# Kernel tuning notes

Hardware: AMD Instinct MI355X
Metric: run time of the kernel (lower is better)

## Reference

```python
import jax, jax.numpy as jnp
import numpy as np

N = 8192
IN_DIM = 512
OUT_DIM = 64
ALPHA = 0.2  # LeakyReLU negative slope
NEG_FILL = -9e15


def setup_inputs() -> dict:
    key = jax.random.key(0)
    k1, k2, k3, k4 = jax.random.split(key, 4)
    features = jax.random.normal(k1, (N, IN_DIM), dtype=jnp.float32)
    adj = jax.random.randint(k2, (N, N), 0, 2, dtype=jnp.int32)
    # xavier_normal with gain 1.414 ~ sqrt(2)
    W = jax.random.normal(k3, (IN_DIM, OUT_DIM), dtype=jnp.float32) * (1.414 * np.sqrt(2.0 / (IN_DIM + OUT_DIM)))
    a = jax.random.normal(k4, (2 * OUT_DIM, 1), dtype=jnp.float32) * (1.414 * np.sqrt(2.0 / (2 * OUT_DIM + 1)))
    return {"features": features, "adj": adj, "W": W, "a": a}


def reference(features, adj, W, a):
    h = features @ W                      # [N, OUT_DIM]
    h1 = h @ a[:OUT_DIM, :]               # [N, 1]
    h2 = h @ a[OUT_DIM:, :]               # [N, 1]
    e = h1 + h2.T                         # [N, N] broadcast add
    e = jnp.where(e > 0, e, ALPHA * e)    # LeakyReLU
    scores = jnp.where(adj > 0, e, NEG_FILL)
    attention = jax.nn.softmax(scores, axis=-1)
    out = attention @ h                   # [N, OUT_DIM]
    out = jax.nn.elu(out)                 # concat=True branch
    return out
```

## Files before the change

### kernel.cpp

```cpp
#include <hip/hip_runtime.h>
#include <hip/hip_bf16.h>

#define N 8192
#define IN_DIM 512
#define OUT_DIM 64
#define ALPHA 0.2f
#define LOG2E 1.44269504f

typedef __hip_bfloat16 bf16;
typedef __attribute__((ext_vector_type(8))) short bf16x8;
typedef __attribute__((ext_vector_type(4))) float f32x4;
typedef __attribute__((ext_vector_type(4))) int   int4v;
typedef __attribute__((ext_vector_type(4))) float float4v;

__device__ __forceinline__ float u2f(unsigned short u) {
    union { unsigned int i; float f; } c; c.i = ((unsigned int)u) << 16; return c.f;
}

__device__ __forceinline__ uint2 splitpack2(float f0, float f1) {
    unsigned u0 = __float_as_uint(f0), u1 = __float_as_uint(f1);
    unsigned h0 = u0 & 0xFFFF0000u, h1 = u1 & 0xFFFF0000u;
    float l0 = f0 - __uint_as_float(h0);
    float l1 = f1 - __uint_as_float(h1);
    uint2 r;
    r.x = (h0 >> 16) | h1;
    r.y = (__float_as_uint(l0) >> 16) | (__float_as_uint(l1) & 0xFFFF0000u);
    return r;
}

__device__ __forceinline__ bf16x8 as_bf16x8(int a, int b, int c, int d) {
    union { int4v i; bf16x8 b; } u;
    u.i = (int4v){a, b, c, d};
    return u.b;
}

__device__ __forceinline__ unsigned fenc(float f) {
    unsigned u = __float_as_uint(f);
    return (u & 0x80000000u) ? ~u : (u | 0x80000000u);
}
__device__ __forceinline__ float fdec(unsigned e) {
    return (e & 0x80000000u) ? __uint_as_float(e & 0x7FFFFFFFu) : __uint_as_float(~e);
}

__device__ __forceinline__ int4v ntload4(const int* p) {
    return __builtin_nontemporal_load((const int4v*)p);
}

__global__ __launch_bounds__(256) void k_prep(const unsigned short* __restrict__ feat_u16,
                                              const void* __restrict__ Wv,
                                              int* __restrict__ flag,
                                              unsigned short* __restrict__ WT_hi,
                                              unsigned short* __restrict__ WT_lo,
                                              unsigned* __restrict__ h2enc) {
    __shared__ int sflag;
    int tid = threadIdx.x;
    if (tid < 64) {
        float v = u2f(feat_u16[2 * tid]);
        float av = fabsf(v);
        int ok = (v == 0.f) || (av > 1e-8f && av < 1e8f);
        unsigned long long m = __ballot(ok);
        if (tid == 0) sflag = (__popcll(m) >= 48) ? 1 : 0;
    }
    __syncthreads();
    int isbf = sflag;
    if (blockIdx.x == 0 && tid == 0) { *flag = isbf; *h2enc = fenc(-3e38f); }
    int idx = blockIdx.x * 256 + tid;
    int k = idx >> 6, c = idx & 63;
    float w = isbf ? u2f(((const unsigned short*)Wv)[idx]) : ((const float*)Wv)[idx];
    unsigned u = __float_as_uint(w);
    unsigned hi = u & 0xFFFF0000u;
    float lo = w - __uint_as_float(hi);
    WT_hi[c * IN_DIM + k] = (unsigned short)(hi >> 16);
    WT_lo[c * IN_DIM + k] = (unsigned short)(__float_as_uint(lo) >> 16);
}

__global__ __launch_bounds__(256) void k_h(const void* __restrict__ featv,
                                           const unsigned short* __restrict__ WT_hi,
                                           const unsigned short* __restrict__ WT_lo,
                                           const void* __restrict__ av,
                                           const int* __restrict__ flag,
                                           float* __restrict__ h1,
                                           float* __restrict__ h2,
                                           unsigned short* __restrict__ hT_hi,
                                           unsigned short* __restrict__ hT_lo,
                                           unsigned* __restrict__ h2enc) {
    __shared__ float C[16][66];
    const int tid = threadIdx.x;
    const int wave = tid >> 6;
    const int lane = tid & 63;
    const int rsub = lane & 15;
    const int g = lane >> 4;
    const int wrow0 = blockIdx.x * 16;
    const int isbf = *flag;

    f32x4 acc0 = {0.f,0.f,0.f,0.f}, acc1 = {0.f,0.f,0.f,0.f};
    f32x4 acc2 = {0.f,0.f,0.f,0.f}, acc3 = {0.f,0.f,0.f,0.f};

    const int kbeg = wave * (IN_DIM / 4);
    for (int k0 = kbeg; k0 < kbeg + IN_DIM / 4; k0 += 32) {
        const int ka = k0 + g * 8;
        bf16x8 Ah, Al;
        if (isbf) {
            Ah = *(const bf16x8*)((const unsigned short*)featv + (size_t)(wrow0 + rsub) * IN_DIM + ka);
            Al = as_bf16x8(0, 0, 0, 0);
        } else {
            const float* fp = (const float*)featv + (size_t)(wrow0 + rsub) * IN_DIM + ka;
            float4v f0 = *(const float4v*)fp;
            float4v f1 = *(const float4v*)(fp + 4);
            uint2 q0 = splitpack2(f0[0], f0[1]);
            uint2 q1 = splitpack2(f0[2], f0[3]);
            uint2 q2 = splitpack2(f1[0], f1[1]);
            uint2 q3 = splitpack2(f1[2], f1[3]);
            Ah = as_bf16x8((int)q0.x, (int)q1.x, (int)q2.x, (int)q3.x);
            Al = as_bf16x8((int)q0.y, (int)q1.y, (int)q2.y, (int)q3.y);
        }
        const unsigned short* wh = WT_hi + (size_t)rsub * IN_DIM + ka;
        const unsigned short* wl = WT_lo + (size_t)rsub * IN_DIM + ka;
        bf16x8 B0h = *(const bf16x8*)(wh);
        bf16x8 B1h = *(const bf16x8*)(wh + 16 * IN_DIM);
        bf16x8 B2h = *(const bf16x8*)(wh + 32 * IN_DIM);
        bf16x8 B3h = *(const bf16x8*)(wh + 48 * IN_DIM);
        bf16x8 B0l = *(const bf16x8*)(wl);
        bf16x8 B1l = *(const bf16x8*)(wl + 16 * IN_DIM);
        bf16x8 B2l = *(const bf16x8*)(wl + 32 * IN_DIM);
        bf16x8 B3l = *(const bf16x8*)(wl + 48 * IN_DIM);

        acc0 = __builtin_amdgcn_mfma_f32_16x16x32_bf16(Ah, B0h, acc0, 0, 0, 0);
        acc1 = __builtin_amdgcn_mfma_f32_16x16x32_bf16(Ah, B1h, acc1, 0, 0, 0);
        acc2 = __builtin_amdgcn_mfma_f32_16x16x32_bf16(Ah, B2h, acc2, 0, 0, 0);
        acc3 = __builtin_amdgcn_mfma_f32_16x16x32_bf16(Ah, B3h, acc3, 0, 0, 0);
        acc0 = __builtin_amdgcn_mfma_f32_16x16x32_bf16(Ah, B0l, acc0, 0, 0, 0);
        acc1 = __builtin_amdgcn_mfma_f32_16x16x32_bf16(Ah, B1l, acc1, 0, 0, 0);
        acc2 = __builtin_amdgcn_mfma_f32_16x16x32_bf16(Ah, B2l, acc2, 0, 0, 0);
        acc3 = __builtin_amdgcn_mfma_f32_16x16x32_bf16(Ah, B3l, acc3, 0, 0, 0);
        acc0 = __builtin_amdgcn_mfma_f32_16x16x32_bf16(Al, B0h, acc0, 0, 0, 0);
        acc1 = __builtin_amdgcn_mfma_f32_16x16x32_bf16(Al, B1h, acc1, 0, 0, 0);
        acc2 = __builtin_amdgcn_mfma_f32_16x16x32_bf16(Al, B2h, acc2, 0, 0, 0);
        acc3 = __builtin_amdgcn_mfma_f32_16x16x32_bf16(Al, B3h, acc3, 0, 0, 0);
    }

    if (wave == 0) {
#pragma unroll
        for (int r = 0; r < 4; ++r) {
            C[g * 4 + r][rsub]      = acc0[r];
            C[g * 4 + r][16 + rsub] = acc1[r];
            C[g * 4 + r][32 + rsub] = acc2[r];
            C[g * 4 + r][48 + rsub] = acc3[r];
        }
    }
    __syncthreads();
#pragma unroll
    for (int w2 = 1; w2 < 4; ++w2) {
        if (wave == w2) {
#pragma unroll
            for (int r = 0; r < 4; ++r) {
                C[g * 4 + r][rsub]      += acc0[r];
                C[g * 4 + r][16 + rsub] += acc1[r];
                C[g * 4 + r][32 + rsub] += acc2[r];
                C[g * 4 + r][48 + rsub] += acc3[r];
            }
        }
        __syncthreads();
    }

    {
        int c = tid >> 2;
        int r0 = (tid & 3) * 4;
        int a = wrow0 + r0;
        int dest = (a & ~31) + 8 * ((a >> 2) & 3) + 4 * ((a >> 4) & 1);
        float v0 = C[r0 + 0][c], v1 = C[r0 + 1][c], v2 = C[r0 + 2][c], v3 = C[r0 + 3][c];
        uint2 s01 = splitpack2(v0, v1);
        uint2 s23 = splitpack2(v2, v3);
        size_t off = (size_t)c * N + dest;
        { uint2 ph; ph.x = s01.x; ph.y = s23.x; *(uint2*)(hT_hi + off) = ph; }
        { uint2 pl; pl.x = s01.y; pl.y = s23.y; *(uint2*)(hT_lo + off) = pl; }
    }

    if (wave == 0 && lane < 16) {
        const float* af = (const float*)av;
        const unsigned short* au = (const unsigned short*)av;
        float s1 = 0.f, s2 = 0.f;
#pragma unroll 8
        for (int c = 0; c < 64; ++c) {
            float a1 = isbf ? u2f(au[c])      : af[c];
            float a2 = isbf ? u2f(au[64 + c]) : af[64 + c];
            float hv = C[lane][c];
            s1 += hv * a1;
            s2 += hv * a2;
        }
        s1 *= LOG2E; s2 *= LOG2E;
        h1[wrow0 + lane] = s1;
        h2[wrow0 + lane] = s2;
        float wm = s2;
#pragma unroll
        for (int off = 8; off; off >>= 1) wm = fmaxf(wm, __shfl_xor(wm, off));
        if (lane == 0) atomicMax(h2enc, fenc(wm));
    }
}

__global__ __launch_bounds__(256, 2) void k_attn(const int* __restrict__ adj,
                                                 const float* __restrict__ h1,
                                                 const float* __restrict__ h2,
                                                 const unsigned short* __restrict__ hT_hi,
                                                 const unsigned short* __restrict__ hT_lo,
                                                 const unsigned* __restrict__ h2enc,
                                                 float* __restrict__ pacc,
                                                 float* __restrict__ plner,
                                                 int klen) {
    __shared__ float accs[64][66];
    __shared__ float lredL[4][64];

    const int wave = threadIdx.x >> 6;
    const int lane = threadIdx.x & 63;
    const int rsub = lane & 15;
    const int g = lane >> 4;
    const int row0 = blockIdx.x * 64;
    const int kbid = blockIdx.y;

    const float h2m = fdec(*h2enc);
    float h1r[4], c0[4];
#pragma unroll
    for (int mt = 0; mt < 4; ++mt) {
        h1r[mt] = h1[row0 + mt * 16 + rsub];
        float u = h1r[mt] + h2m;
        c0[mt] = -fmaxf(u, ALPHA * u);
    }

    f32x4 acc[4][4];
#pragma unroll
    for (int mt = 0; mt < 4; ++mt)
#pragma unroll
        for (int ct = 0; ct < 4; ++ct) acc[mt][ct] = (f32x4){0.f, 0.f, 0.f, 0.f};
    float lacc[4] = {0.f, 0.f, 0.f, 0.f};

    const unsigned short* bph = hT_hi + (size_t)rsub * N;
    const unsigned short* bpl = hT_lo + (size_t)rsub * N;

    const int kbeg = kbid * klen + wave * (klen >> 2);
    const int kend = kbeg + (klen >> 2);
    for (int k0 = kbeg; k0 < kend; k0 += 32) {
        const int kb = k0 + g * 8;
        const int ca = k0 + g * 4;
        const int cb = k0 + 16 + g * 4;

        const unsigned short* bh = bph + kb;
        const unsigned short* bl = bpl + kb;
        bf16x8 B0h = *(const bf16x8*)(bh);
        bf16x8 B1h = *(const bf16x8*)(bh + 16 * (size_t)N);
        bf16x8 B2h = *(const bf16x8*)(bh + 32 * (size_t)N);
        bf16x8 B3h = *(const bf16x8*)(bh + 48 * (size_t)N);
        bf16x8 B0l = *(const bf16x8*)(bl);
        bf16x8 B1l = *(const bf16x8*)(bl + 16 * (size_t)N);
        bf16x8 B2l = *(const bf16x8*)(bl + 32 * (size_t)N);
        bf16x8 B3l = *(const bf16x8*)(bl + 48 * (size_t)N);

        float4v hA = *(const float4v*)(h2 + ca);
        float4v hB = *(const float4v*)(h2 + cb);

#pragma unroll
        for (int mt = 0; mt < 4; ++mt) {
            const size_t arow = (size_t)(row0 + mt * 16 + rsub) * N;
            int4v aj0 = ntload4(adj + arow + ca);
            int4v aj1 = ntload4(adj + arow + cb);

            float w[8];
#pragma unroll
            for (int j = 0; j < 4; ++j) {
                float u = h1r[mt] + hA[j];
                float s = fmaxf(u, ALPHA * u);
                float e = exp2f(s + c0[mt]);
                w[j] = aj0[j] > 0 ? e : 0.f;
            }
#pragma unroll
            for (int j = 0; j < 4; ++j) {
                float u = h1r[mt] + hB[j];
                float s = fmaxf(u, ALPHA * u);
                float e = exp2f(s + c0[mt]);
                w[4 + j] = aj1[j] > 0 ? e : 0.f;
            }
#pragma unroll
            for (int j = 0; j < 8; ++j) lacc[mt] += w[j];

            uint2 p0 = splitpack2(w[0], w[1]);
            uint2 p1 = splitpack2(w[2], w[3]);
            uint2 p2 = splitpack2(w[4], w[5]);
            uint2 p3 = splitpack2(w[6], w[7]);
            bf16x8 Ahi = as_bf16x8((int)p0.x, (int)p1.x, (int)p2.x, (int)p3.x);
            bf16x8 Alo = as_bf16x8((int)p0.y, (int)p1.y, (int)p2.y, (int)p3.y);

            acc[mt][0] = __builtin_amdgcn_mfma_f32_16x16x32_bf16(Ahi, B0h, acc[mt][0], 0, 0, 0);
            acc[mt][1] = __builtin_amdgcn_mfma_f32_16x16x32_bf16(Ahi, B1h, acc[mt][1], 0, 0, 0);
            acc[mt][2] = __builtin_amdgcn_mfma_f32_16x16x32_bf16(Ahi, B2h, acc[mt][2], 0, 0, 0);
            acc[mt][3] = __builtin_amdgcn_mfma_f32_16x16x32_bf16(Ahi, B3h, acc[mt][3], 0, 0, 0);
            acc[mt][0] = __builtin_amdgcn_mfma_f32_16x16x32_bf16(Ahi, B0l, acc[mt][0], 0, 0, 0);
            acc[mt][1] = __builtin_amdgcn_mfma_f32_16x16x32_bf16(Ahi, B1l, acc[mt][1], 0, 0, 0);
            acc[mt][2] = __builtin_amdgcn_mfma_f32_16x16x32_bf16(Ahi, B2l, acc[mt][2], 0, 0, 0);
            acc[mt][3] = __builtin_amdgcn_mfma_f32_16x16x32_bf16(Ahi, B3l, acc[mt][3], 0, 0, 0);
            acc[mt][0] = __builtin_amdgcn_mfma_f32_16x16x32_bf16(Alo, B0h, acc[mt][0], 0, 0, 0);
            acc[mt][1] = __builtin_amdgcn_mfma_f32_16x16x32_bf16(Alo, B1h, acc[mt][1], 0, 0, 0);
            acc[mt][2] = __builtin_amdgcn_mfma_f32_16x16x32_bf16(Alo, B2h, acc[mt][2], 0, 0, 0);
            acc[mt][3] = __builtin_amdgcn_mfma_f32_16x16x32_bf16(Alo, B3h, acc[mt][3], 0, 0, 0);
        }
    }

#pragma unroll
    for (int mt = 0; mt < 4; ++mt) {
        float l = lacc[mt];
        l += __shfl_xor(l, 16);
        l += __shfl_xor(l, 32);
        if (g == 0) lredL[wave][mt * 16 + rsub] = l;
    }

    if (wave == 0) {
#pragma unroll
        for (int mt = 0; mt < 4; ++mt)
#pragma unroll
            for (int ct = 0; ct < 4; ++ct)
#pragma unroll
                for (int r = 0; r < 4; ++r)
                    accs[mt * 16 + g * 4 + r][ct * 16 + rsub] = acc[mt][ct][r];
    }
    __syncthreads();
#pragma unroll
    for (int w2 = 1; w2 < 4; ++w2) {
        if (wave == w2) {
#pragma unroll
            for (int mt = 0; mt < 4; ++mt)
#pragma unroll
                for (int ct = 0; ct < 4; ++ct)
#pragma unroll
                    for (int r = 0; r < 4; ++r)
                        accs[mt * 16 + g * 4 + r][ct * 16 + rsub] += acc[mt][ct][r];
        }
        __syncthreads();
    }

    float* pa = pacc + (size_t)kbid * (N * OUT_DIM);
#pragma unroll
    for (int p = 0; p < 16; ++p) {
        int idx = p * 256 + threadIdx.x;
        int rl = idx >> 6, col = idx & 63;
        pa[(size_t)(row0 + rl) * OUT_DIM + col] = accs[rl][col];
    }
    if (threadIdx.x < 64)
        plner[(size_t)kbid * N + row0 + threadIdx.x] =
            lredL[0][threadIdx.x] + lredL[1][threadIdx.x] + lredL[2][threadIdx.x] + lredL[3][threadIdx.x];
}

__global__ __launch_bounds__(256) void k_out(const float* __restrict__ pacc,
                                             const float* __restrict__ plner,
                                             const int* __restrict__ flag,
                                             void* __restrict__ outv,
                                             int nkb) {
    int idx = blockIdx.x * 256 + threadIdx.x;
    int row = idx >> 6;
    float v = 0.f, l = 0.f;
    for (int kb = 0; kb < nkb; ++kb) {
        v += pacc[(size_t)kb * (N * OUT_DIM) + idx];
        l += plner[(size_t)kb * N + row];
    }
    float o = l > 0.f ? v / l : 0.f;
    o = o > 0.f ? o : exp2f(o * LOG2E) - 1.f;
    if (*flag) ((bf16*)outv)[idx] = __float2bfloat16(o);
    else       ((float*)outv)[idx] = o;
}

extern "C" void kernel_launch(void* const* d_in, const int* in_sizes, int n_in,
                              void* d_out, int out_size, void* d_ws, size_t ws_size,
                              hipStream_t stream) {
    const void* feat = d_in[0];
    const int* adj = (const int*)d_in[1];
    const void* W = d_in[2];
    const void* a = d_in[3];

    char* ws = (char*)d_ws;
    int*      flag  = (int*)(ws);
    unsigned* h2enc = (unsigned*)(ws + 256);
    float* h1       = (float*)(ws + 4096);
    float* h2       = (float*)(ws + 36864);
    unsigned short* hT_hi = (unsigned short*)(ws + 69632);
    unsigned short* hT_lo = (unsigned short*)(ws + 69632 + 1048576);
    unsigned short* WT_hi = (unsigned short*)(ws + 2166784);
    unsigned short* WT_lo = (unsigned short*)(ws + 2166784 + 65536);
    char* dynbase = ws + 2297856;

    size_t cap = ws_size ? ws_size : ((size_t)1 << 30);
    int nkb = 8;
    while (nkb > 1) {
        size_t need = 2297856 + (size_t)nkb * ((size_t)N * OUT_DIM * 4 + (size_t)N * 4);
        if (need <= cap) break;
        nkb >>= 1;
    }
    float* pacc  = (float*)dynbase;
    float* plner = (float*)(dynbase + (size_t)nkb * N * OUT_DIM * 4);

    hipLaunchKernelGGL(k_prep, dim3((IN_DIM * OUT_DIM) / 256), dim3(256), 0, stream,
                       (const unsigned short*)feat, W, flag, WT_hi, WT_lo, h2enc);
    hipLaunchKernelGGL(k_h, dim3(N / 16), dim3(256), 0, stream,
                       feat, WT_hi, WT_lo, a, flag, h1, h2, hT_hi, hT_lo, h2enc);
    hipLaunchKernelGGL(k_attn, dim3(N / 64, nkb), dim3(256), 0, stream,
                       adj, h1, h2, hT_hi, hT_lo, h2enc, pacc, plner, N / nkb);
    hipLaunchKernelGGL(k_out, dim3((N * OUT_DIM) / 256), dim3(256), 0, stream,
                       pacc, plner, flag, d_out, nkb);
}
```

Before: 436.0 us.

## Pack adjacency into bitmask in projection kernel and consume bits in attention

Adds extra blocks to the feature-projection kernel that read the int32 adjacency once and ballot it into a 1-bit-per-entry mask. The attention kernel then stages its rows of the mask in shared memory instead of streaming 4-byte adjacency values from global memory per MFMA step. The hT layout is simplified to plain row order, to match the new column-to-bit mapping. Adjacency is still read in full once, but now in a kernel that overlaps with the projection, and the attention kernel gains LDS usage and a barrier. The number of key splits can no longer drop below four.

```diff
diff --git a/kernel.cpp b/kernel.cpp
--- a/kernel.cpp
+++ b/kernel.cpp
@@ -40,10 +40,6 @@
 }
 __device__ __forceinline__ float fdec(unsigned e) {
     return (e & 0x80000000u) ? __uint_as_float(e & 0x7FFFFFFFu) : __uint_as_float(~e);
-}
-
-__device__ __forceinline__ int4v ntload4(const int* p) {
-    return __builtin_nontemporal_load((const int4v*)p);
 }
 
 __global__ __launch_bounds__(256) void k_prep(const unsigned short* __restrict__ feat_u16,
@@ -74,20 +70,38 @@
     WT_lo[c * IN_DIM + k] = (unsigned short)(__float_as_uint(lo) >> 16);
 }
 
-__global__ __launch_bounds__(256) void k_h(const void* __restrict__ featv,
-                                           const unsigned short* __restrict__ WT_hi,
-                                           const unsigned short* __restrict__ WT_lo,
-                                           const void* __restrict__ av,
-                                           const int* __restrict__ flag,
-                                           float* __restrict__ h1,
-                                           float* __restrict__ h2,
-                                           unsigned short* __restrict__ hT_hi,
-                                           unsigned short* __restrict__ hT_lo,
-                                           unsigned* __restrict__ h2enc) {
+__global__ __launch_bounds__(256) void k_hp(const void* __restrict__ featv,
+                                            const unsigned short* __restrict__ WT_hi,
+                                            const unsigned short* __restrict__ WT_lo,
+                                            const void* __restrict__ av,
+                                            const int* __restrict__ flag,
+                                            float* __restrict__ h1,
+                                            float* __restrict__ h2,
+                                            unsigned short* __restrict__ hT_hi,
+                                            unsigned short* __restrict__ hT_lo,
+                                            unsigned* __restrict__ h2enc,
+                                            const int* __restrict__ adj,
+                                            unsigned* __restrict__ abits) {
     __shared__ float C[16][66];
     const int tid = threadIdx.x;
     const int wave = tid >> 6;
     const int lane = tid & 63;
+
+    if (blockIdx.x >= N / 16) {
+        const size_t base = (size_t)(blockIdx.x - N / 16) * 512;
+#pragma unroll 4
+        for (int it = 0; it < 128; ++it) {
+            size_t chunk = base + (size_t)it * 4 + wave;
+            int v = adj[chunk * 64 + lane];
+            unsigned long long m = __ballot(v > 0);
+            if (lane == 0) {
+                uint2 p; p.x = (unsigned)m; p.y = (unsigned)(m >> 32);
+                *(uint2*)(abits + chunk * 2) = p;
+            }
+        }
+        return;
+    }
+
     const int rsub = lane & 15;
     const int g = lane >> 4;
     const int wrow0 = blockIdx.x * 16;
@@ -166,12 +180,10 @@
     {
         int c = tid >> 2;
         int r0 = (tid & 3) * 4;
-        int a = wrow0 + r0;
-        int dest = (a & ~31) + 8 * ((a >> 2) & 3) + 4 * ((a >> 4) & 1);
         float v0 = C[r0 + 0][c], v1 = C[r0 + 1][c], v2 = C[r0 + 2][c], v3 = C[r0 + 3][c];
         uint2 s01 = splitpack2(v0, v1);
         uint2 s23 = splitpack2(v2, v3);
-        size_t off = (size_t)c * N + dest;
+        size_t off = (size_t)c * N + wrow0 + r0;
         { uint2 ph; ph.x = s01.x; ph.y = s23.x; *(uint2*)(hT_hi + off) = ph; }
         { uint2 pl; pl.x = s01.y; pl.y = s23.y; *(uint2*)(hT_lo + off) = pl; }
     }
@@ -198,7 +210,7 @@
     }
 }
 
-__global__ __launch_bounds__(256, 2) void k_attn(const int* __restrict__ adj,
+__global__ __launch_bounds__(256, 2) void k_attn(const unsigned* __restrict__ abits,
                                                  const float* __restrict__ h1,
                                                  const float* __restrict__ h2,
                                                  const unsigned short* __restrict__ hT_hi,
@@ -209,6 +221,7 @@
                                                  int klen) {
     __shared__ float accs[64][66];
     __shared__ float lredL[4][64];
+    __shared__ unsigned msk[64][65];
 
     const int wave = threadIdx.x >> 6;
     const int lane = threadIdx.x & 63;
@@ -217,6 +230,13 @@
     const int row0 = blockIdx.x * 64;
     const int kbid = blockIdx.y;
 
+    const int wpr = klen >> 5;
+    const int wsh = 31 - __clz(wpr);
+    for (int i = threadIdx.x; i < 64 * wpr; i += 256) {
+        int r = i >> wsh, w = i & (wpr - 1);
+        msk[r][w] = abits[(size_t)(row0 + r) * (N / 32) + (size_t)kbid * wpr + w];
+    }
+
     const float h2m = fdec(*h2enc);
     float h1r[4], c0[4];
 #pragma unroll
@@ -236,12 +256,14 @@
     const unsigned short* bph = hT_hi + (size_t)rsub * N;
     const unsigned short* bpl = hT_lo + (size_t)rsub * N;
 
+    __syncthreads();
+
     const int kbeg = kbid * klen + wave * (klen >> 2);
     const int kend = kbeg + (klen >> 2);
+    const int sh = g * 8;
     for (int k0 = kbeg; k0 < kend; k0 += 32) {
         const int kb = k0 + g * 8;
-        const int ca = k0 + g * 4;
-        const int cb = k0 + 16 + g * 4;
+        const int wi = (k0 - kbid * klen) >> 5;
 
         const unsigned short* bh = bph + kb;
         const unsigned short* bl = bpl + kb;
@@ -254,14 +276,12 @@
         bf16x8 B2l = *(const bf16x8*)(bl + 32 * (size_t)N);
         bf16x8 B3l = *(const bf16x8*)(bl + 48 * (size_t)N);
 
-        float4v hA = *(const float4v*)(h2 + ca);
-        float4v hB = *(const float4v*)(h2 + cb);
+        float4v hA = *(const float4v*)(h2 + kb);
+        float4v hB = *(const float4v*)(h2 + kb + 4);
 
 #pragma unroll
         for (int mt = 0; mt < 4; ++mt) {
-            const size_t arow = (size_t)(row0 + mt * 16 + rsub) * N;
-            int4v aj0 = ntload4(adj + arow + ca);
-            int4v aj1 = ntload4(adj + arow + cb);
+            const unsigned mask = msk[mt * 16 + rsub][wi];
 
             float w[8];
 #pragma unroll
@@ -269,14 +289,14 @@
                 float u = h1r[mt] + hA[j];
                 float s = fmaxf(u, ALPHA * u);
                 float e = exp2f(s + c0[mt]);
-                w[j] = aj0[j] > 0 ? e : 0.f;
+                w[j] = ((mask >> (sh + j)) & 1u) ? e : 0.f;
             }
 #pragma unroll
             for (int j = 0; j < 4; ++j) {
                 float u = h1r[mt] + hB[j];
                 float s = fmaxf(u, ALPHA * u);
                 float e = exp2f(s + c0[mt]);
-                w[4 + j] = aj1[j] > 0 ? e : 0.f;
+                w[4 + j] = ((mask >> (sh + 4 + j)) & 1u) ? e : 0.f;
             }
 #pragma unroll
             for (int j = 0; j < 8; ++j) lacc[mt] += w[j];
@@ -382,12 +402,13 @@
     unsigned short* hT_lo = (unsigned short*)(ws + 69632 + 1048576);
     unsigned short* WT_hi = (unsigned short*)(ws + 2166784);
     unsigned short* WT_lo = (unsigned short*)(ws + 2166784 + 65536);
-    char* dynbase = ws + 2297856;
+    unsigned* abits = (unsigned*)(ws + 2297856);
+    char* dynbase = ws + 2297856 + (size_t)N * (N / 8);
 
     size_t cap = ws_size ? ws_size : ((size_t)1 << 30);
     int nkb = 8;
-    while (nkb > 1) {
-        size_t need = 2297856 + (size_t)nkb * ((size_t)N * OUT_DIM * 4 + (size_t)N * 4);
+    while (nkb > 4) {
+        size_t need = (size_t)(dynbase - ws) + (size_t)nkb * ((size_t)N * OUT_DIM * 4 + (size_t)N * 4);
         if (need <= cap) break;
         nkb >>= 1;
     }
@@ -396,10 +417,10 @@
 
     hipLaunchKernelGGL(k_prep, dim3((IN_DIM * OUT_DIM) / 256), dim3(256), 0, stream,
                        (const unsigned short*)feat, W, flag, WT_hi, WT_lo, h2enc);
-    hipLaunchKernelGGL(k_h, dim3(N / 16), dim3(256), 0, stream,
-                       feat, WT_hi, WT_lo, a, flag, h1, h2, hT_hi, hT_lo, h2enc);
+    hipLaunchKernelGGL(k_hp, dim3(N / 16 + 2048), dim3(256), 0, stream,
+                       feat, WT_hi, WT_lo, a, flag, h1, h2, hT_hi, hT_lo, h2enc, adj, abits);
     hipLaunchKernelGGL(k_attn, dim3(N / 64, nkb), dim3(256), 0, stream,
-                       adj, h1, h2, hT_hi, hT_lo, h2enc, pacc, plner, N / nkb);
+                       abits, h1, h2, hT_hi, hT_lo, h2enc, pacc, plner, N / nkb);
     hipLaunchKernelGGL(k_out, dim3((N * OUT_DIM) / 256), dim3(256), 0, stream,
                        pacc, plner, flag, d_out, nkb);
 }
```

Result: slower. 512.4 us (+17.5%).

## Prefetch adjacency into shared-memory bitmasks with coalesced loads and ballots

Applied to the files above, without the earlier changes.

Each block now reads its adjacency tile up front with fully coalesced row loads, packs it into per-row bitmasks in shared memory with wave ballots, and then tests mask bits in the MFMA loop. This replaces the strided nontemporal int4 loads issued inside the compute loop. The hT layout permutation is removed, so h and h2 columns map contiguously to the MFMA k-index. The K split grows to 16 partitions (minimum 8), which adds partial-sum traffic and shared-memory use, and it introduces a load phase that does not overlap with compute.

```diff
diff --git a/kernel.cpp b/kernel.cpp
--- a/kernel.cpp
+++ b/kernel.cpp
@@ -40,10 +40,6 @@
 }
 __device__ __forceinline__ float fdec(unsigned e) {
     return (e & 0x80000000u) ? __uint_as_float(e & 0x7FFFFFFFu) : __uint_as_float(~e);
-}
-
-__device__ __forceinline__ int4v ntload4(const int* p) {
-    return __builtin_nontemporal_load((const int4v*)p);
 }
 
 __global__ __launch_bounds__(256) void k_prep(const unsigned short* __restrict__ feat_u16,
@@ -166,12 +162,10 @@
     {
         int c = tid >> 2;
         int r0 = (tid & 3) * 4;
-        int a = wrow0 + r0;
-        int dest = (a & ~31) + 8 * ((a >> 2) & 3) + 4 * ((a >> 4) & 1);
         float v0 = C[r0 + 0][c], v1 = C[r0 + 1][c], v2 = C[r0 + 2][c], v3 = C[r0 + 3][c];
         uint2 s01 = splitpack2(v0, v1);
         uint2 s23 = splitpack2(v2, v3);
-        size_t off = (size_t)c * N + dest;
+        size_t off = (size_t)c * N + wrow0 + r0;
         { uint2 ph; ph.x = s01.x; ph.y = s23.x; *(uint2*)(hT_hi + off) = ph; }
         { uint2 pl; pl.x = s01.y; pl.y = s23.y; *(uint2*)(hT_lo + off) = pl; }
     }
@@ -209,13 +203,47 @@
                                                  int klen) {
     __shared__ float accs[64][66];
     __shared__ float lredL[4][64];
-
+    __shared__ unsigned msk[64][34];
     const int wave = threadIdx.x >> 6;
     const int lane = threadIdx.x & 63;
     const int rsub = lane & 15;
     const int g = lane >> 4;
     const int row0 = blockIdx.x * 64;
     const int kbid = blockIdx.y;
+    const int colbase = kbid * klen;
+
+    for (int r = wave * 16; r < wave * 16 + 16; ++r) {
+        const int* p = adj + (size_t)(row0 + r) * N + colbase;
+        for (int cb = 0; cb < klen; cb += 512) {
+            int v0 = p[cb + 0 * 64 + lane];
+            int v1 = p[cb + 1 * 64 + lane];
+            int v2 = p[cb + 2 * 64 + lane];
+            int v3 = p[cb + 3 * 64 + lane];
+            int v4 = p[cb + 4 * 64 + lane];
+            int v5 = p[cb + 5 * 64 + lane];
+            int v6 = p[cb + 6 * 64 + lane];
+            int v7 = p[cb + 7 * 64 + lane];
+            unsigned long long m0 = __ballot(v0 > 0);
+            unsigned long long m1 = __ballot(v1 > 0);
+            unsigned long long m2 = __ballot(v2 > 0);
+            unsigned long long m3 = __ballot(v3 > 0);
+            unsigned long long m4 = __ballot(v4 > 0);
+            unsigned long long m5 = __ballot(v5 > 0);
+            unsigned long long m6 = __ballot(v6 > 0);
+            unsigned long long m7 = __ballot(v7 > 0);
+            if (lane == 0) {
+                int w0 = cb >> 5;
+                { uint2 q; q.x = (unsigned)m0; q.y = (unsigned)(m0 >> 32); *(uint2*)&msk[r][w0 + 0]  = q; }
+                { uint2 q; q.x = (unsigned)m1; q.y = (unsigned)(m1 >> 32); *(uint2*)&msk[r][w0 + 2]  = q; }
+                { uint2 q; q.x = (unsigned)m2; q.y = (unsigned)(m2 >> 32); *(uint2*)&msk[r][w0 + 4]  = q; }
+                { uint2 q; q.x = (unsigned)m3; q.y = (unsigned)(m3 >> 32); *(uint2*)&msk[r][w0 + 6]  = q; }
+                { uint2 q; q.x = (unsigned)m4; q.y = (unsigned)(m4 >> 32); *(uint2*)&msk[r][w0 + 8]  = q; }
+                { uint2 q; q.x = (unsigned)m5; q.y = (unsigned)(m5 >> 32); *(uint2*)&msk[r][w0 + 10] = q; }
+                { uint2 q; q.x = (unsigned)m6; q.y = (unsigned)(m6 >> 32); *(uint2*)&msk[r][w0 + 12] = q; }
+                { uint2 q; q.x = (unsigned)m7; q.y = (unsigned)(m7 >> 32); *(uint2*)&msk[r][w0 + 14] = q; }
+            }
+        }
+    }
 
     const float h2m = fdec(*h2enc);
     float h1r[4], c0[4];
@@ -236,12 +264,14 @@
     const unsigned short* bph = hT_hi + (size_t)rsub * N;
     const unsigned short* bpl = hT_lo + (size_t)rsub * N;
 
-    const int kbeg = kbid * klen + wave * (klen >> 2);
+    __syncthreads();
+
+    const int kbeg = colbase + wave * (klen >> 2);
     const int kend = kbeg + (klen >> 2);
+    const int sh = g * 8;
     for (int k0 = kbeg; k0 < kend; k0 += 32) {
         const int kb = k0 + g * 8;
-        const int ca = k0 + g * 4;
-        const int cb = k0 + 16 + g * 4;
+        const int wi = (k0 - colbase) >> 5;
 
         const unsigned short* bh = bph + kb;
         const unsigned short* bl = bpl + kb;
@@ -254,14 +284,12 @@
         bf16x8 B2l = *(const bf16x8*)(bl + 32 * (size_t)N);
         bf16x8 B3l = *(const bf16x8*)(bl + 48 * (size_t)N);
 
-        float4v hA = *(const float4v*)(h2 + ca);
-        float4v hB = *(const float4v*)(h2 + cb);
+        float4v hA = *(const float4v*)(h2 + kb);
+        float4v hB = *(const float4v*)(h2 + kb + 4);
 
 #pragma unroll
         for (int mt = 0; mt < 4; ++mt) {
-            const size_t arow = (size_t)(row0 + mt * 16 + rsub) * N;
-            int4v aj0 = ntload4(adj + arow + ca);
-            int4v aj1 = ntload4(adj + arow + cb);
+            const unsigned mask = msk[mt * 16 + rsub][wi];
 
             float w[8];
 #pragma unroll
@@ -269,14 +297,14 @@
                 float u = h1r[mt] + hA[j];
                 float s = fmaxf(u, ALPHA * u);
                 float e = exp2f(s + c0[mt]);
-                w[j] = aj0[j] > 0 ? e : 0.f;
+                w[j] = ((mask >> (sh + j)) & 1u) ? e : 0.f;
             }
 #pragma unroll
             for (int j = 0; j < 4; ++j) {
                 float u = h1r[mt] + hB[j];
                 float s = fmaxf(u, ALPHA * u);
                 float e = exp2f(s + c0[mt]);
-                w[4 + j] = aj1[j] > 0 ? e : 0.f;
+                w[4 + j] = ((mask >> (sh + 4 + j)) & 1u) ? e : 0.f;
             }
 #pragma unroll
             for (int j = 0; j < 8; ++j) lacc[mt] += w[j];
@@ -385,9 +413,9 @@
     char* dynbase = ws + 2297856;
 
     size_t cap = ws_size ? ws_size : ((size_t)1 << 30);
-    int nkb = 8;
-    while (nkb > 1) {
-        size_t need = 2297856 + (size_t)nkb * ((size_t)N * OUT_DIM * 4 + (size_t)N * 4);
+    int nkb = 16;
+    while (nkb > 8) {
+        size_t need = (size_t)(dynbase - ws) + (size_t)nkb * ((size_t)N * OUT_DIM * 4 + (size_t)N * 4);
         if (need <= cap) break;
         nkb >>= 1;
     }
```

Result: slower. 453.8 us (+4.1%).
